# Optimization experiments

Hardware: AMD Instinct MI355X
Metric: run time of the kernel (lower is better)

The kernel has to match this reference:

```python
import jax, jax.numpy as jnp
import numpy as np

B, N_IN, N_OUT, DEG = 128, 16384, 8192, 64
N_EDGES = N_OUT * DEG


def setup_inputs() -> dict:
    key = jax.random.key(0)
    k_x, k_src, k_dst, k_w = jax.random.split(key, 4)
    x = jax.random.normal(k_x, (B, N_IN), dtype=jnp.float32)
    # Ragged connectivity flattened to a CSR-like edge list:
    # edge_src[e] -> input feature index, edge_dst[e] -> output unit index.
    edge_src = jax.random.randint(k_src, (N_EDGES,), 0, N_IN, dtype=jnp.int64)
    edge_dst = jnp.sort(jax.random.randint(k_dst, (N_EDGES,), 0, N_OUT, dtype=jnp.int64))
    w = jax.random.normal(k_w, (N_EDGES,), dtype=jnp.float32) * 0.05  # one weight per edge
    bias = jnp.zeros((N_OUT,), dtype=jnp.float32)
    return {"x": x, "w": w, "bias": bias, "edge_src": edge_src, "edge_dst": edge_dst}


def reference(x, w, bias, edge_src, edge_dst):
    # Equivalent to: for each output j, y[:, j] = relu(x[:, edges_j] @ w_j + bias[j])
    # Vectorized as a single gather + weighted scatter-add over the flat edge list.
    n_out = bias.shape[0]
    gathered = x[:, edge_src] * w  # [B, E]
    y = jnp.zeros((x.shape[0], n_out), dtype=x.dtype).at[:, edge_dst].add(gathered)
    return jax.nn.relu(y + bias)
```

## Files before the change

kernel.cpp:

```cpp
#include <hip/hip_runtime.h>
#include <hip/hip_fp16.h>

#define B_DIM   128
#define N_IN    16384
#define N_OUT   8192
#define N_EDGES (N_OUT * 64)

#define J_BLK    8
#define THREADS  (J_BLK * 64)
#define JGROUPS  (N_OUT / J_BLK)

__device__ __forceinline__ int lower_bound_dev(const int* __restrict__ a, int n, int v) {
    int lo = 0, hi = n;
    while (lo < hi) {
        int mid = (lo + hi) >> 1;
        if (a[mid] < v) lo = mid + 1; else hi = mid;
    }
    return lo;
}

__global__ void build_rowptr_kernel(const int* __restrict__ dst, int* __restrict__ rp) {
    const int e = blockIdx.x * blockDim.x + threadIdx.x;
    if (e >= N_EDGES) return;
    const int d     = dst[e];
    const int dprev = (e == 0) ? -1 : dst[e - 1];
    for (int j = dprev + 1; j <= d; ++j) rp[j] = e;
    if (e == N_EDGES - 1)
        for (int j = d + 1; j <= N_OUT; ++j) rp[j] = N_EDGES;
}

__global__ __launch_bounds__(256) void transpose_h_kernel(const float* __restrict__ x,
                                                          __half* __restrict__ xTh) {
    __shared__ float tile[64][33];
    const int i0 = blockIdx.x * 32;
    const int b0 = blockIdx.y * 64;
    const int tx = threadIdx.x;
    const int ty = threadIdx.y;
#pragma unroll
    for (int r = 0; r < 64; r += 8)
        tile[ty + r][tx] = x[(size_t)(b0 + ty + r) * N_IN + (i0 + tx)];
    __syncthreads();
    __half2* out = (__half2*)xTh;
#pragma unroll
    for (int rr = 0; rr < 4; ++rr) {
        const int il = rr * 8 + ty;
        const float a = tile[2 * tx][il];
        const float b = tile[2 * tx + 1][il];
        out[(size_t)(i0 + il) * (B_DIM / 2) + (b0 >> 1) + tx] = __floats2half2_rn(a, b);
    }
}

__global__ __launch_bounds__(THREADS, 8) void sparse_layer_h(
        const __half* __restrict__ xTh, const float* __restrict__ w,
        const float* __restrict__ bias, const int* __restrict__ src,
        const int* __restrict__ rp, float* __restrict__ y) {
    __shared__ float tile[J_BLK][132];

    const int tid  = threadIdx.x;
    const int wid  = tid >> 6;
    const int lane = tid & 63;
    const int slot = lane >> 4;
    const int bl   = lane & 15;
    const int j0   = blockIdx.x * J_BLK;
    const int j    = j0 + wid;

    const int e0 = __builtin_amdgcn_readfirstlane(rp[j]);
    const int e1 = __builtin_amdgcn_readfirstlane(rp[j + 1]);

    float acc[8] = {0.f, 0.f, 0.f, 0.f, 0.f, 0.f, 0.f, 0.f};
    const char* xbase = (const char*)xTh + bl * 16;

#pragma unroll 4
    for (int e = e0; e < e1; e += 4) {
        const int  ee    = e + slot;
        const bool valid = ee < e1;
        const int  ec    = valid ? ee : e0;
        const int  s     = src[ec];
        const float wt   = valid ? w[ec] : 0.f;
        const float4 raw = *(const float4*)(xbase + (size_t)s * (B_DIM * 2));
        const __half2* hp = (const __half2*)&raw;
#pragma unroll
        for (int q = 0; q < 4; ++q) {
            const float2 f = __half22float2(hp[q]);
            acc[2 * q]     = fmaf(f.x, wt, acc[2 * q]);
            acc[2 * q + 1] = fmaf(f.y, wt, acc[2 * q + 1]);
        }
    }

#pragma unroll
    for (int m = 16; m <= 32; m <<= 1)
#pragma unroll
        for (int q = 0; q < 8; ++q) acc[q] += __shfl_xor(acc[q], m, 64);

    if (slot == 0) {
#pragma unroll
        for (int q = 0; q < 8; ++q) tile[wid][8 * bl + q] = acc[q];
    }
    __syncthreads();

#pragma unroll
    for (int i = tid; i < B_DIM * J_BLK; i += THREADS) {
        const int bb = i >> 3;
        const int jj = i & (J_BLK - 1);
        const float v = tile[jj][bb] + bias[j0 + jj];
        y[(size_t)bb * N_OUT + (j0 + jj)] = fmaxf(v, 0.f);
    }
}

__global__ __launch_bounds__(THREADS) void sparse_layer_fallback(
        const float* __restrict__ x, const float* __restrict__ w,
        const float* __restrict__ bias, const int* __restrict__ src,
        const int* __restrict__ dst, float* __restrict__ y) {
    __shared__ float tile[J_BLK][130];
    __shared__ int   srp[J_BLK + 1];

    const int tid  = threadIdx.x;
    const int wid  = tid >> 6;
    const int lane = tid & 63;
    const int j0   = blockIdx.x * J_BLK;

    if (tid <= J_BLK) srp[tid] = lower_bound_dev(dst, N_EDGES, j0 + tid);
    __syncthreads();

    const int e0 = srp[wid], e1 = srp[wid + 1];
    const int b0 = lane * 2;
    float acc0 = 0.f, acc1 = 0.f;
    for (int e = e0; e < e1; ++e) {
        const int   s  = src[e];
        const float wt = w[e];
        acc0 = fmaf(x[(size_t)b0 * N_IN + s], wt, acc0);
        acc1 = fmaf(x[(size_t)(b0 + 1) * N_IN + s], wt, acc1);
    }
    tile[wid][b0]     = acc0;
    tile[wid][b0 + 1] = acc1;
    __syncthreads();
#pragma unroll
    for (int i = tid; i < B_DIM * J_BLK; i += THREADS) {
        const int bb = i >> 3;
        const int jj = i & (J_BLK - 1);
        const float v = tile[jj][bb] + bias[j0 + jj];
        y[(size_t)bb * N_OUT + (j0 + jj)] = fmaxf(v, 0.f);
    }
}

extern "C" void kernel_launch(void* const* d_in, const int* in_sizes, int n_in,
                              void* d_out, int out_size, void* d_ws, size_t ws_size,
                              hipStream_t stream) {
    const float* x    = (const float*)d_in[0];
    const float* w    = (const float*)d_in[1];
    const float* bias = (const float*)d_in[2];
    const int*   esrc = (const int*)d_in[3];
    const int*   edst = (const int*)d_in[4];
    float*       y    = (float*)d_out;

    const size_t RP_BYTES = (size_t)(N_OUT + 1) * sizeof(int);
    const size_t XT_OFF   = 65536;
    const size_t XT_BYTES = (size_t)N_IN * B_DIM * sizeof(__half);

    const bool has_ws = ws_size >= XT_OFF + XT_BYTES && ws_size >= RP_BYTES;

    int*    rp  = (int*)d_ws;
    __half* xTh = (__half*)((char*)d_ws + XT_OFF);

    if (has_ws) {
        build_rowptr_kernel<<<(N_EDGES + 255) / 256, 256, 0, stream>>>(edst, rp);
        transpose_h_kernel<<<dim3(N_IN / 32, B_DIM / 64), dim3(32, 8), 0, stream>>>(x, xTh);
        sparse_layer_h<<<dim3(JGROUPS), THREADS, 0, stream>>>(xTh, w, bias, esrc, rp, y);
    } else {
        sparse_layer_fallback<<<dim3(N_OUT / J_BLK), THREADS, 0, stream>>>(x, w, bias, esrc, edst, y);
    }
}
```

Before: 86.77 us.

## Pack edge src/weight into int2 metadata and broadcast per-wave via shuffles

The prep kernel now also writes an interleaved (byte offset, weight) int2 array for every edge. The main kernel loads 64 edges' metadata with one coalesced load per wave and hands each edge to its lane slot with __shfl. This replaces the per-slot scalar src/w loads and the index multiply in the inner loop, and adds a fully unrolled path for full 64-edge chunks. In exchange it writes and reads an extra 4MB of metadata, spends extra shuffles per edge, and lowers the launch-bounds occupancy hint from 8 to 4.

```diff
diff --git a/kernel.cpp b/kernel.cpp
--- a/kernel.cpp
+++ b/kernel.cpp
@@ -19,14 +19,19 @@
     return lo;
 }
 
-__global__ void build_rowptr_kernel(const int* __restrict__ dst, int* __restrict__ rp) {
-    const int e = blockIdx.x * blockDim.x + threadIdx.x;
+__global__ __launch_bounds__(256) void prep_kernel(const int* __restrict__ dst,
+                                                   const int* __restrict__ src,
+                                                   const float* __restrict__ w,
+                                                   int* __restrict__ rp,
+                                                   int2* __restrict__ meta) {
+    const int e = blockIdx.x * 256 + threadIdx.x;
     if (e >= N_EDGES) return;
     const int d     = dst[e];
     const int dprev = (e == 0) ? -1 : dst[e - 1];
     for (int j = dprev + 1; j <= d; ++j) rp[j] = e;
     if (e == N_EDGES - 1)
         for (int j = d + 1; j <= N_OUT; ++j) rp[j] = N_EDGES;
+    meta[e] = make_int2(src[e] * (B_DIM * 2), __float_as_int(w[e]));
 }
 
 __global__ __launch_bounds__(256) void transpose_h_kernel(const float* __restrict__ x,
@@ -50,10 +55,25 @@
     }
 }
 
-__global__ __launch_bounds__(THREADS, 8) void sparse_layer_h(
-        const __half* __restrict__ xTh, const float* __restrict__ w,
-        const float* __restrict__ bias, const int* __restrict__ src,
-        const int* __restrict__ rp, float* __restrict__ y) {
+#define GATHER_FMA(K)                                                              \
+    do {                                                                           \
+        const int   idx = 4 * (K) + slot;                                          \
+        const int   o   = __shfl(moff, idx, 64);                                   \
+        const float wt  = __int_as_float(__shfl(mw, idx, 64));                     \
+        const float4 raw = *(const float4*)(xb + (size_t)(unsigned)o);             \
+        const __half2* hp = (const __half2*)&raw;                                  \
+        _Pragma("unroll")                                                          \
+        for (int q = 0; q < 4; ++q) {                                              \
+            const float2 f = __half22float2(hp[q]);                                \
+            acc[2 * q]     = fmaf(f.x, wt, acc[2 * q]);                            \
+            acc[2 * q + 1] = fmaf(f.y, wt, acc[2 * q + 1]);                        \
+        }                                                                          \
+    } while (0)
+
+__global__ __launch_bounds__(THREADS, 4) void sparse_layer_h2(
+        const __half* __restrict__ xTh, const float* __restrict__ bias,
+        const int2* __restrict__ meta, const int* __restrict__ rp,
+        float* __restrict__ y) {
     __shared__ float tile[J_BLK][132];
 
     const int tid  = threadIdx.x;
@@ -68,29 +88,27 @@
     const int e1 = __builtin_amdgcn_readfirstlane(rp[j + 1]);
 
     float acc[8] = {0.f, 0.f, 0.f, 0.f, 0.f, 0.f, 0.f, 0.f};
-    const char* xbase = (const char*)xTh + bl * 16;
+    const char* xb = (const char*)xTh + bl * 16;
 
-#pragma unroll 4
-    for (int e = e0; e < e1; e += 4) {
-        const int  ee    = e + slot;
-        const bool valid = ee < e1;
-        const int  ec    = valid ? ee : e0;
-        const int  s     = src[ec];
-        const float wt   = valid ? w[ec] : 0.f;
-        const float4 raw = *(const float4*)(xbase + (size_t)s * (B_DIM * 2));
-        const __half2* hp = (const __half2*)&raw;
+    for (int base = e0; base < e1; base += 64) {
+        const int n = min(64, e1 - base);
+        int moff = 0, mw = 0;
+        if (lane < n) {
+            const int2 m = meta[base + lane];
+            moff = m.x; mw = m.y;
+        }
+        if (n == 64) {
 #pragma unroll
-        for (int q = 0; q < 4; ++q) {
-            const float2 f = __half22float2(hp[q]);
-            acc[2 * q]     = fmaf(f.x, wt, acc[2 * q]);
-            acc[2 * q + 1] = fmaf(f.y, wt, acc[2 * q + 1]);
+            for (int k = 0; k < 16; ++k) GATHER_FMA(k);
+        } else {
+            for (int k = 0; 4 * k < n; ++k) GATHER_FMA(k);
         }
     }
 
 #pragma unroll
-    for (int m = 16; m <= 32; m <<= 1)
+    for (int m_ = 16; m_ <= 32; m_ <<= 1)
 #pragma unroll
-        for (int q = 0; q < 8; ++q) acc[q] += __shfl_xor(acc[q], m, 64);
+        for (int q = 0; q < 8; ++q) acc[q] += __shfl_xor(acc[q], m_, 64);
 
     if (slot == 0) {
 #pragma unroll
@@ -153,19 +171,21 @@
     const int*   edst = (const int*)d_in[4];
     float*       y    = (float*)d_out;
 
-    const size_t RP_BYTES = (size_t)(N_OUT + 1) * sizeof(int);
-    const size_t XT_OFF   = 65536;
+    const size_t META_OFF = 65536;
+    const size_t META_BYTES = (size_t)N_EDGES * sizeof(int2);
+    const size_t XT_OFF   = META_OFF + META_BYTES;
     const size_t XT_BYTES = (size_t)N_IN * B_DIM * sizeof(__half);
 
-    const bool has_ws = ws_size >= XT_OFF + XT_BYTES && ws_size >= RP_BYTES;
+    const bool has_ws = ws_size >= XT_OFF + XT_BYTES;
 
-    int*    rp  = (int*)d_ws;
-    __half* xTh = (__half*)((char*)d_ws + XT_OFF);
+    int*    rp   = (int*)d_ws;
+    int2*   meta = (int2*)((char*)d_ws + META_OFF);
+    __half* xTh  = (__half*)((char*)d_ws + XT_OFF);
 
     if (has_ws) {
-        build_rowptr_kernel<<<(N_EDGES + 255) / 256, 256, 0, stream>>>(edst, rp);
+        prep_kernel<<<dim3((N_EDGES + 255) / 256), 256, 0, stream>>>(edst, esrc, w, rp, meta);
         transpose_h_kernel<<<dim3(N_IN / 32, B_DIM / 64), dim3(32, 8), 0, stream>>>(x, xTh);
-        sparse_layer_h<<<dim3(JGROUPS), THREADS, 0, stream>>>(xTh, w, bias, esrc, rp, y);
+        sparse_layer_h2<<<dim3(JGROUPS), THREADS, 0, stream>>>(xTh, bias, meta, rp, y);
     } else {
         sparse_layer_fallback<<<dim3(N_OUT / J_BLK), THREADS, 0, stream>>>(x, w, bias, esrc, edst, y);
     }
```

Result: slower. 90.60 us (+4.4%).

## Sort each output row's edges by source index before gathering

Applied to the files above, without the earlier changes.

Adds a per-row bitonic sort kernel that reorders each output unit's edges (source index and weight together) by source index, then feeds the sorted arrays to the gather kernel. The aim is more locality in gathers of transposed x rows across the four lanes and across successive iterations. The cost is an extra kernel launch plus reading and writing about 4 MB of edge data on every call, and a larger workspace requirement. Rows with more than 128 edges are copied unsorted, so results stay correct.

```diff
diff --git a/kernel.cpp b/kernel.cpp
--- a/kernel.cpp
+++ b/kernel.cpp
@@ -29,6 +29,55 @@
         for (int j = d + 1; j <= N_OUT; ++j) rp[j] = N_EDGES;
 }
 
+__global__ __launch_bounds__(512) void sort_kernel(const int* __restrict__ src,
+                                                   const float* __restrict__ w,
+                                                   const int* __restrict__ rp,
+                                                   int* __restrict__ ssrc,
+                                                   float* __restrict__ sw) {
+    const int gw   = (blockIdx.x * 512 + threadIdx.x) >> 6;
+    const int lane = threadIdx.x & 63;
+    if (gw >= N_OUT) return;
+    const int e0 = rp[gw], e1 = rp[gw + 1];
+    const int n  = e1 - e0;
+    if (n <= 0) return;
+    if (n > 128) {
+        for (int e = e0 + lane; e < e1; e += 64) { ssrc[e] = src[e]; sw[e] = w[e]; }
+        return;
+    }
+    int   k0 = 0x7FFFFFFF, k1 = 0x7FFFFFFF;
+    float w0 = 0.f,        w1 = 0.f;
+    if (lane < n)      { k0 = (src[e0 + lane]      << 7) | lane;        w0 = w[e0 + lane]; }
+    if (lane + 64 < n) { k1 = (src[e0 + 64 + lane] << 7) | (64 + lane); w1 = w[e0 + 64 + lane]; }
+
+#pragma unroll
+    for (int k = 2; k <= 128; k <<= 1) {
+#pragma unroll
+        for (int jj = 64; jj > 0; jj >>= 1) {
+            if (jj >= k) continue;
+            if (jj == 64) {
+                const bool swp = k1 < k0;
+                const int   lo = swp ? k1 : k0, hi = swp ? k0 : k1;
+                const float wl = swp ? w1 : w0, wh = swp ? w0 : w1;
+                k0 = lo; k1 = hi; w0 = wl; w1 = wh;
+            } else {
+                const bool lower = (lane & jj) == 0;
+                const bool up0   = ((lane & k) == 0);
+                const bool up1   = (((lane + 64) & k) == 0);
+                int   pk0 = __shfl_xor(k0, jj, 64);
+                float pw0 = __shfl_xor(w0, jj, 64);
+                const bool take0 = (lower == up0) ? (pk0 < k0) : (pk0 > k0);
+                if (take0) { k0 = pk0; w0 = pw0; }
+                int   pk1 = __shfl_xor(k1, jj, 64);
+                float pw1 = __shfl_xor(w1, jj, 64);
+                const bool take1 = (lower == up1) ? (pk1 < k1) : (pk1 > k1);
+                if (take1) { k1 = pk1; w1 = pw1; }
+            }
+        }
+    }
+    if (lane < n)      { ssrc[e0 + lane]      = k0 >> 7; sw[e0 + lane]      = w0; }
+    if (lane + 64 < n) { ssrc[e0 + 64 + lane] = k1 >> 7; sw[e0 + 64 + lane] = w1; }
+}
+
 __global__ __launch_bounds__(256) void transpose_h_kernel(const float* __restrict__ x,
                                                           __half* __restrict__ xTh) {
     __shared__ float tile[64][33];
@@ -51,8 +100,8 @@
 }
 
 __global__ __launch_bounds__(THREADS, 8) void sparse_layer_h(
-        const __half* __restrict__ xTh, const float* __restrict__ w,
-        const float* __restrict__ bias, const int* __restrict__ src,
+        const __half* __restrict__ xTh, const float* __restrict__ sw,
+        const float* __restrict__ bias, const int* __restrict__ ssrc,
         const int* __restrict__ rp, float* __restrict__ y) {
     __shared__ float tile[J_BLK][132];
 
@@ -75,8 +124,8 @@
         const int  ee    = e + slot;
         const bool valid = ee < e1;
         const int  ec    = valid ? ee : e0;
-        const int  s     = src[ec];
-        const float wt   = valid ? w[ec] : 0.f;
+        const int  s     = ssrc[ec];
+        const float wt   = valid ? sw[ec] : 0.f;
         const float4 raw = *(const float4*)(xbase + (size_t)s * (B_DIM * 2));
         const __half2* hp = (const __half2*)&raw;
 #pragma unroll
@@ -153,19 +202,25 @@
     const int*   edst = (const int*)d_in[4];
     float*       y    = (float*)d_out;
 
-    const size_t RP_BYTES = (size_t)(N_OUT + 1) * sizeof(int);
-    const size_t XT_OFF   = 65536;
+    const size_t SSRC_OFF = 65536;
+    const size_t SSRC_BY  = (size_t)N_EDGES * sizeof(int);
+    const size_t SW_OFF   = SSRC_OFF + SSRC_BY;
+    const size_t SW_BY    = (size_t)N_EDGES * sizeof(float);
+    const size_t XT_OFF   = SW_OFF + SW_BY;
     const size_t XT_BYTES = (size_t)N_IN * B_DIM * sizeof(__half);
 
-    const bool has_ws = ws_size >= XT_OFF + XT_BYTES && ws_size >= RP_BYTES;
-
-    int*    rp  = (int*)d_ws;
-    __half* xTh = (__half*)((char*)d_ws + XT_OFF);
+    const bool has_ws = ws_size >= XT_OFF + XT_BYTES;
+
+    int*    rp   = (int*)d_ws;
+    int*    ssrc = (int*)((char*)d_ws + SSRC_OFF);
+    float*  sw   = (float*)((char*)d_ws + SW_OFF);
+    __half* xTh  = (__half*)((char*)d_ws + XT_OFF);
 
     if (has_ws) {
         build_rowptr_kernel<<<(N_EDGES + 255) / 256, 256, 0, stream>>>(edst, rp);
+        sort_kernel<<<dim3((N_OUT * 64 + 511) / 512), 512, 0, stream>>>(esrc, w, rp, ssrc, sw);
         transpose_h_kernel<<<dim3(N_IN / 32, B_DIM / 64), dim3(32, 8), 0, stream>>>(x, xTh);
-        sparse_layer_h<<<dim3(JGROUPS), THREADS, 0, stream>>>(xTh, w, bias, esrc, rp, y);
+        sparse_layer_h<<<dim3(JGROUPS), THREADS, 0, stream>>>(xTh, sw, bias, ssrc, rp, y);
     } else {
         sparse_layer_fallback<<<dim3(N_OUT / J_BLK), THREADS, 0, stream>>>(x, w, bias, esrc, edst, y);
     }
```

After: 97.28 us. 1.12x slower.
